# Performance work log

Measured on AMD Instinct MI355X. Metric: run time of the kernel, lower is better.

The kernel has to match this reference:

```python
import jax, jax.numpy as jnp
import numpy as np

N_NODES = 256
DIM = 128
N_LAYERS = 3
LN_EPS = 1e-5


def setup_inputs() -> dict:
    key = jax.random.key(0)
    ks = jax.random.split(key, 8)
    B = 2048
    node_features = jax.random.normal(ks[0], (B, N_NODES, DIM), dtype=jnp.float32)
    A_logits_pos = jax.random.normal(ks[1], (N_NODES, N_NODES), dtype=jnp.float32) * 0.01
    A_logits_neg = jax.random.normal(ks[2], (N_NODES, N_NODES), dtype=jnp.float32) * 0.01
    # per-layer Linear weights, torch layout (out_dim, in_dim); all dims are 128
    scale = 1.0 / np.sqrt(DIM)
    W_pos = jax.random.uniform(ks[3], (N_LAYERS, DIM, DIM), jnp.float32, -scale, scale)
    W_neg = jax.random.uniform(ks[4], (N_LAYERS, DIM, DIM), jnp.float32, -scale, scale)
    ln_g = jnp.ones((N_LAYERS, DIM), jnp.float32)
    ln_b = jnp.zeros((N_LAYERS, DIM), jnp.float32)
    ro_g = jnp.ones((DIM,), jnp.float32)
    ro_b = jnp.zeros((DIM,), jnp.float32)
    return {"node_features": node_features, "A_logits_pos": A_logits_pos,
            "A_logits_neg": A_logits_neg, "W_pos": W_pos, "W_neg": W_neg,
            "ln_g": ln_g, "ln_b": ln_b, "ro_g": ro_g, "ro_b": ro_b}


def _layernorm(x, g, b):
    mu = jnp.mean(x, axis=-1, keepdims=True)
    var = jnp.var(x, axis=-1, keepdims=True)
    return (x - mu) * jax.lax.rsqrt(var + LN_EPS) * g + b


def reference(node_features, A_logits_pos, A_logits_neg, W_pos, W_neg, ln_g, ln_b, ro_g, ro_b):
    # soft signed adjacency with hard-mask split (mask is non-differentiable)
    A_p = jax.nn.sigmoid(A_logits_pos)
    A_n = jax.nn.sigmoid(A_logits_neg)
    mask = (A_p > A_n).astype(A_p.dtype)
    A_pos = A_p * mask
    A_neg = A_n * (1.0 - mask)

    H = node_features  # (B, N, D)
    for l in range(N_LAYERS):
        agg_pos = jnp.einsum('uv,bvd->bud', A_pos, H)
        agg_neg = jnp.einsum('uv,bvd->bud', A_neg, H)
        # torch Linear: x @ W.T ; GELU is exact (erf) by default in torch
        out = jax.nn.gelu(jnp.einsum('bud,od->buo', agg_pos, W_pos[l])
                          - jnp.einsum('bud,od->buo', agg_neg, W_neg[l]),
                          approximate=False)
        H = _layernorm(out, ln_g[l], ln_b[l])  # dropout = identity in eval

    h_G = jnp.mean(H, axis=1)  # (B, D) readout
    return _layernorm(h_G, ro_g, ro_b)
```

## Files before the change

### kernel.cpp

```cpp
#include <hip/hip_runtime.h>
#include <math.h>


typedef float  f32x4  __attribute__((ext_vector_type(4)));
typedef float  f32x16 __attribute__((ext_vector_type(16)));
typedef short  s16x8  __attribute__((ext_vector_type(8)));
typedef __bf16 bf16x8 __attribute__((ext_vector_type(8)));

#define GOFF 65536

#define LDS_BARRIER() asm volatile("s_waitcnt lgkmcnt(0)\n\ts_barrier" ::: "memory")

__device__ __forceinline__ unsigned short f2bf(float f) {
  __bf16 h = (__bf16)f;
  return __builtin_bit_cast(unsigned short, h);
}
__device__ __forceinline__ float bf2f(unsigned short h) {
  return __builtin_bit_cast(float, (unsigned int)h << 16);
}
__device__ __forceinline__ unsigned short f2bf_rne(float f) {
  unsigned int u = __builtin_bit_cast(unsigned int, f);
  u = (u + 0x7fffu + ((u >> 16) & 1u)) >> 16;
  return (unsigned short)u;
}

__device__ __forceinline__ float gelu_fast(float x) {
  float z = fabsf(x) * 0.70710678f;
  float t = __builtin_amdgcn_rcpf(1.f + 0.3275911f * z);
  float p = t * (0.254829592f + t * (-0.284496736f + t * (1.421413741f +
            t * (-1.453152027f + t * 1.061405429f))));
  float e = __builtin_expf(-z * z);
  float erfv = 1.f - p * e;
  erfv = (x < 0.f) ? -erfv : erfv;
  return 0.5f * x * (1.f + erfv);
}

__device__ __forceinline__ int haddr(int v, int d) {
  return v * 256 + ((d * 2) ^ ((v & 15) << 4));
}
__device__ __forceinline__ int gaddr(int o, int vr) {
  return GOFF + o * 80 + vr * 2;
}

#define MFMA32(a, b, c) __builtin_amdgcn_mfma_f32_32x32x16_bf16( \
    __builtin_bit_cast(bf16x8, (a)), __builtin_bit_cast(bf16x8, (b)), (c), 0, 0, 0)

__global__ void prep_kernel(const float* __restrict__ alp, const float* __restrict__ aln,
                            const float* __restrict__ wp,  const float* __restrict__ wn,
                            unsigned short* __restrict__ A3, unsigned short* __restrict__ W3) {
  int idx = blockIdx.x * 512 + threadIdx.x;
  if (idx < 131072) {
    int j = idx & 7, lane = (idx >> 3) & 63, vt = (idx >> 9) & 15,
        ut = (idx >> 13) & 7, h = (idx >> 16) & 1;
    int u = ut * 32 + (lane & 31);
    int v = vt * 16 + (lane >> 5) * 8 + j;
    int s = u * 256 + v;
    float ap = 1.f / (1.f + expf(-alp[s]));
    float an = 1.f / (1.f + expf(-aln[s]));
    bool  m  = ap > an;
    float val = h ? (m ? 0.f : -an) : (m ? ap : 0.f);
    A3[idx] = f2bf_rne(val);
  } else {
    int k = idx - 131072;
    int j = k & 7, lane = (k >> 3) & 63, kt = (k >> 9) & 7,
        ot = (k >> 12) & 3, hw = (k >> 14);
    int o = ot * 32 + (lane & 31);
    int d = kt * 16 + (lane >> 5) * 8 + j;
    const float* src = (hw & 1) ? wn : wp;
    W3[k] = f2bf_rne(src[(hw >> 1) * 16384 + o * 128 + d]);
  }
}

__global__ __launch_bounds__(256, 2) void gnn_kernel(
    const float* __restrict__ X,
    const unsigned short* __restrict__ A3,
    const unsigned short* __restrict__ W3,
    const float* __restrict__ ln_g, const float* __restrict__ ln_b,
    const float* __restrict__ ro_g, const float* __restrict__ ro_b,
    float* __restrict__ out) {
  extern __shared__ char smem[];
  const int tid  = threadIdx.x;
  const int wid  = tid >> 6;
  const int lane = tid & 63;
  const int l31  = lane & 31;
  const int hi   = lane >> 5;
  const int b    = blockIdx.x;

  {
    const float4* Xb = (const float4*)(X + (size_t)b * 256 * 128);
#pragma unroll 8
    for (int i = 0; i < 32; ++i) {
      int idx = tid + i * 256;
      int v = idx >> 5, d = (idx & 31) * 4;
      float4 f = Xb[idx];
      ushort4 p;
      p.x = f2bf(f.x); p.y = f2bf(f.y); p.z = f2bf(f.z); p.w = f2bf(f.w);
      *(ushort4*)(smem + haddr(v, d)) = p;
    }
  }
  __syncthreads();

  f32x16 acc[2][4];
  for (int l = 0; l < 3; ++l) {
#pragma unroll
    for (int mt = 0; mt < 2; ++mt)
#pragma unroll
      for (int nt = 0; nt < 4; ++nt)
#pragma unroll
        for (int r = 0; r < 16; ++r) acc[mt][nt][r] = 0.f;

    for (int h = 0; h < 2; ++h) {
      const unsigned short* Wb = W3 + (size_t)(((l * 2 + h) * 4 + wid) * 8) * 512;
      const unsigned short* Ab = A3 + (size_t)((h * 8 + wid * 2) * 16) * 512;

      s16x8 wreg[8];
#pragma unroll
      for (int kt = 0; kt < 8; ++kt)
        wreg[kt] = *(const s16x8*)(Wb + (size_t)kt * 512 + lane * 8);

      for (int c = 0; c < 8; ++c) {
        s16x8 pa[4];
#pragma unroll
        for (int kt = 0; kt < 2; ++kt) {
          pa[kt * 2 + 0] = *(const s16x8*)(Ab + (size_t)(0 * 16 + c * 2 + kt) * 512 + lane * 8);
          pa[kt * 2 + 1] = *(const s16x8*)(Ab + (size_t)(1 * 16 + c * 2 + kt) * 512 + lane * 8);
        }

        f32x16 g0;
#pragma unroll
        for (int r = 0; r < 16; ++r) g0[r] = 0.f;
        const int v0 = c * 32 + l31;
        __builtin_amdgcn_s_setprio(1);
#pragma unroll
        for (int kt = 0; kt < 8; ++kt) {
          s16x8 ha = *(const s16x8*)(smem + haddr(v0, kt * 16 + hi * 8));
          g0 = MFMA32(ha, wreg[kt], g0);
        }
        __builtin_amdgcn_s_setprio(0);
        LDS_BARRIER();
        {
          const int og = wid * 32 + l31;
#pragma unroll
          for (int rq = 0; rq < 4; ++rq) {
            int vr = rq * 8 + hi * 4;
            ushort4 p;
            p.x = f2bf(g0[rq*4+0]); p.y = f2bf(g0[rq*4+1]);
            p.z = f2bf(g0[rq*4+2]); p.w = f2bf(g0[rq*4+3]);
            *(ushort4*)(smem + gaddr(og, vr)) = p;
          }
        }
        LDS_BARRIER();

        __builtin_amdgcn_s_setprio(1);
#pragma unroll
        for (int kt = 0; kt < 2; ++kt) {
#pragma unroll
          for (int nt = 0; nt < 4; ++nt) {
            s16x8 bf = *(const s16x8*)(smem + gaddr(nt * 32 + l31, kt * 16 + hi * 8));
            acc[0][nt] = MFMA32(pa[kt * 2 + 0], bf, acc[0][nt]);
            acc[1][nt] = MFMA32(pa[kt * 2 + 1], bf, acc[1][nt]);
          }
        }
        __builtin_amdgcn_s_setprio(0);
      }
    }

    {
      float lg[4], lb[4];
#pragma unroll
      for (int nt = 0; nt < 4; ++nt) {
        lg[nt] = ln_g[l * 128 + nt * 32 + l31];
        lb[nt] = ln_b[l * 128 + nt * 32 + l31];
      }
#pragma unroll
      for (int mt = 0; mt < 2; ++mt)
#pragma unroll
        for (int r = 0; r < 16; ++r) {
          float x0 = gelu_fast(acc[mt][0][r]);
          float x1 = gelu_fast(acc[mt][1][r]);
          float x2 = gelu_fast(acc[mt][2][r]);
          float x3 = gelu_fast(acc[mt][3][r]);
          acc[mt][0][r] = x0; acc[mt][1][r] = x1;
          acc[mt][2][r] = x2; acc[mt][3][r] = x3;
          float s1 = x0 + x1 + x2 + x3;
          float s2 = x0 * x0 + x1 * x1 + x2 * x2 + x3 * x3;
#pragma unroll
          for (int m = 1; m < 32; m <<= 1) {
            s1 += __shfl_xor(s1, m);
            s2 += __shfl_xor(s2, m);
          }
          float mu  = s1 * (1.f / 128.f);
          float var = s2 * (1.f / 128.f) - mu * mu;
          float rs  = rsqrtf(var + 1e-5f);
          int u = wid * 64 + mt * 32 + (r & 3) + 8 * ((r >> 2) & 3) + 4 * hi;
#pragma unroll
          for (int nt = 0; nt < 4; ++nt) {
            float y = (acc[mt][nt][r] - mu) * rs * lg[nt] + lb[nt];
            *(unsigned short*)(smem + haddr(u, nt * 32 + l31)) = f2bf(y);
          }
        }
    }
    __syncthreads();
  }

  {
    int d   = tid & 127;
    int grp = tid >> 7;
    float s = 0.f;
    for (int v = grp * 128; v < grp * 128 + 128; ++v)
      s += bf2f(*(const unsigned short*)(smem + haddr(v, d)));
    float* red = (float*)(smem + GOFF);
    red[grp * 128 + d] = s;
    __syncthreads();
    if (tid < 128) {
      red[256 + tid] = (red[tid] + red[128 + tid]) * (1.f / 256.f);
    }
    __syncthreads();
    if (tid < 64) {
      float a  = red[256 + tid];
      float b2 = red[256 + 64 + tid];
      float s1 = a + b2, s2 = a * a + b2 * b2;
#pragma unroll
      for (int m = 1; m < 64; m <<= 1) {
        s1 += __shfl_xor(s1, m);
        s2 += __shfl_xor(s2, m);
      }
      float mu  = s1 * (1.f / 128.f);
      float var = s2 * (1.f / 128.f) - mu * mu;
      float rs  = rsqrtf(var + 1e-5f);
      out[(size_t)b * 128 + tid]      = (a  - mu) * rs * ro_g[tid]      + ro_b[tid];
      out[(size_t)b * 128 + 64 + tid] = (b2 - mu) * rs * ro_g[64 + tid] + ro_b[64 + tid];
    }
  }
}

extern "C" void kernel_launch(void* const* d_in, const int* in_sizes, int n_in,
                              void* d_out, int out_size, void* d_ws, size_t ws_size,
                              hipStream_t stream) {
  const float* X   = (const float*)d_in[0];
  const float* alp = (const float*)d_in[1];
  const float* aln = (const float*)d_in[2];
  const float* wp  = (const float*)d_in[3];
  const float* wn  = (const float*)d_in[4];
  const float* lng = (const float*)d_in[5];
  const float* lnb = (const float*)d_in[6];
  const float* rog = (const float*)d_in[7];
  const float* rob = (const float*)d_in[8];
  float* out = (float*)d_out;

  unsigned short* A3 = (unsigned short*)d_ws;
  unsigned short* W3 = A3 + 131072;

  (void)hipFuncSetAttribute(reinterpret_cast<const void*>(gnn_kernel),
                            hipFuncAttributeMaxDynamicSharedMemorySize, 75776);

  prep_kernel<<<448, 512, 0, stream>>>(alp, aln, wp, wn, A3, W3);
  gnn_kernel<<<2048, 256, 75776, stream>>>(X, A3, W3, lng, lnb, rog, rob, out);
}
```

Measured before the change: 630.5 us.

## Double-buffer G tile in LDS to halve barriers per chunk

After: 710.3 us. 1.13x slower.

```diff
diff --git a/kernel.cpp b/kernel.cpp
--- a/kernel.cpp
+++ b/kernel.cpp
@@ -38,8 +38,8 @@
 __device__ __forceinline__ int haddr(int v, int d) {
   return v * 256 + ((d * 2) ^ ((v & 15) << 4));
 }
-__device__ __forceinline__ int gaddr(int o, int vr) {
-  return GOFF + o * 80 + vr * 2;
+__device__ __forceinline__ int gaddr(int buf, int o, int vr) {
+  return GOFF + buf * 8192 + o * 64 + ((vr * 2) ^ ((o & 3) << 4));
 }
 
 #define MFMA32(a, b, c) __builtin_amdgcn_mfma_f32_32x32x16_bf16( \
@@ -118,7 +118,8 @@
       for (int kt = 0; kt < 8; ++kt)
         wreg[kt] = *(const s16x8*)(Wb + (size_t)kt * 512 + lane * 8);
 
-      for (int c = 0; c < 8; ++c) {
+      for (int cp = 0; cp < 4; ++cp) {
+        const int c = cp * 2;
         s16x8 pa[4];
 #pragma unroll
         for (int kt = 0; kt < 2; ++kt) {
@@ -129,14 +130,16 @@
         f32x16 g0;
 #pragma unroll
         for (int r = 0; r < 16; ++r) g0[r] = 0.f;
-        const int v0 = c * 32 + l31;
-        __builtin_amdgcn_s_setprio(1);
-#pragma unroll
-        for (int kt = 0; kt < 8; ++kt) {
-          s16x8 ha = *(const s16x8*)(smem + haddr(v0, kt * 16 + hi * 8));
-          g0 = MFMA32(ha, wreg[kt], g0);
-        }
-        __builtin_amdgcn_s_setprio(0);
+        {
+          const int v0 = c * 32 + l31;
+          __builtin_amdgcn_s_setprio(1);
+#pragma unroll
+          for (int kt = 0; kt < 8; ++kt) {
+            s16x8 ha = *(const s16x8*)(smem + haddr(v0, kt * 16 + hi * 8));
+            g0 = MFMA32(ha, wreg[kt], g0);
+          }
+          __builtin_amdgcn_s_setprio(0);
+        }
         LDS_BARRIER();
         {
           const int og = wid * 32 + l31;
@@ -146,7 +149,30 @@
             ushort4 p;
             p.x = f2bf(g0[rq*4+0]); p.y = f2bf(g0[rq*4+1]);
             p.z = f2bf(g0[rq*4+2]); p.w = f2bf(g0[rq*4+3]);
-            *(ushort4*)(smem + gaddr(og, vr)) = p;
+            *(ushort4*)(smem + gaddr(0, og, vr)) = p;
+          }
+        }
+#pragma unroll
+        for (int r = 0; r < 16; ++r) g0[r] = 0.f;
+        {
+          const int v0 = (c + 1) * 32 + l31;
+          __builtin_amdgcn_s_setprio(1);
+#pragma unroll
+          for (int kt = 0; kt < 8; ++kt) {
+            s16x8 ha = *(const s16x8*)(smem + haddr(v0, kt * 16 + hi * 8));
+            g0 = MFMA32(ha, wreg[kt], g0);
+          }
+          __builtin_amdgcn_s_setprio(0);
+        }
+        {
+          const int og = wid * 32 + l31;
+#pragma unroll
+          for (int rq = 0; rq < 4; ++rq) {
+            int vr = rq * 8 + hi * 4;
+            ushort4 p;
+            p.x = f2bf(g0[rq*4+0]); p.y = f2bf(g0[rq*4+1]);
+            p.z = f2bf(g0[rq*4+2]); p.w = f2bf(g0[rq*4+3]);
+            *(ushort4*)(smem + gaddr(1, og, vr)) = p;
           }
         }
         LDS_BARRIER();
@@ -156,9 +182,20 @@
         for (int kt = 0; kt < 2; ++kt) {
 #pragma unroll
           for (int nt = 0; nt < 4; ++nt) {
-            s16x8 bf = *(const s16x8*)(smem + gaddr(nt * 32 + l31, kt * 16 + hi * 8));
+            s16x8 bf = *(const s16x8*)(smem + gaddr(0, nt * 32 + l31, kt * 16 + hi * 8));
             acc[0][nt] = MFMA32(pa[kt * 2 + 0], bf, acc[0][nt]);
             acc[1][nt] = MFMA32(pa[kt * 2 + 1], bf, acc[1][nt]);
+          }
+        }
+#pragma unroll
+        for (int kt = 0; kt < 2; ++kt) {
+          s16x8 a0 = *(const s16x8*)(Ab + (size_t)(0 * 16 + (c + 1) * 2 + kt) * 512 + lane * 8);
+          s16x8 a1 = *(const s16x8*)(Ab + (size_t)(1 * 16 + (c + 1) * 2 + kt) * 512 + lane * 8);
+#pragma unroll
+          for (int nt = 0; nt < 4; ++nt) {
+            s16x8 bf = *(const s16x8*)(smem + gaddr(1, nt * 32 + l31, kt * 16 + hi * 8));
+            acc[0][nt] = MFMA32(a0, bf, acc[0][nt]);
+            acc[1][nt] = MFMA32(a1, bf, acc[1][nt]);
           }
         }
         __builtin_amdgcn_s_setprio(0);
@@ -252,8 +289,8 @@
   unsigned short* W3 = A3 + 131072;
 
   (void)hipFuncSetAttribute(reinterpret_cast<const void*>(gnn_kernel),
-                            hipFuncAttributeMaxDynamicSharedMemorySize, 75776);
+                            hipFuncAttributeMaxDynamicSharedMemorySize, 81920);
 
   prep_kernel<<<448, 512, 0, stream>>>(alp, aln, wp, wn, A3, W3);
-  gnn_kernel<<<2048, 256, 75776, stream>>>(X, A3, W3, lng, lnb, rog, rob, out);
-}
+  gnn_kernel<<<2048, 256, 81920, stream>>>(X, A3, W3, lng, lnb, rog, rob, out);
+}
```
